# Kernel tuning notes

Measured on AMD Instinct MI355X. Metric: run time of the kernel, lower is better.

The kernel has to match this reference:

```python
import jax, jax.numpy as jnp
import numpy as np

EMBD_DIM = 768
NUM_HEADS = 12
DEPTH = EMBD_DIM // NUM_HEADS


def setup_inputs() -> dict:
    key = jax.random.key(0)
    ks = jax.random.split(key, 8)
    B, S, D = 4, 2048, EMBD_DIM
    scale = 1.0 / np.sqrt(D)
    return {
        "q": jax.random.normal(ks[0], (B, S, D), dtype=jnp.float32),
        "k": jax.random.normal(ks[1], (B, S, D), dtype=jnp.float32),
        "v": jax.random.normal(ks[2], (B, S, D), dtype=jnp.float32),
        # torch nn.Linear stores weight as [out, in]; y = x @ W.T
        "wq": jax.random.normal(ks[3], (D, D), dtype=jnp.float32) * scale,
        "wk": jax.random.normal(ks[4], (D, D), dtype=jnp.float32) * scale,
        "wv": jax.random.normal(ks[5], (D, D), dtype=jnp.float32) * scale,
        "wd": jax.random.normal(ks[6], (D, D), dtype=jnp.float32) * scale,
        "bd": jax.random.normal(ks[7], (D,), dtype=jnp.float32) * 0.01,
    }


def _split_heads(x):
    B, S, _ = x.shape
    return x.reshape(B, S, NUM_HEADS, DEPTH).transpose(0, 2, 1, 3)  # [B,H,S,depth]


def reference(q, k, v, wq, wk, wv, wd, bd):
    B, S, D = q.shape
    qh = _split_heads(q @ wq.T)
    kh = _split_heads(k @ wk.T)
    vh = _split_heads(v @ wv.T)
    scale = jnp.sqrt(jnp.float32(DEPTH))
    logits = jnp.einsum("bhqd,bhkd->bhqk", qh, kh) / scale  # [B,H,S,S]
    attn = jax.nn.softmax(logits, axis=-1)
    ctx = jnp.einsum("bhqk,bhkd->bhqd", attn, vh)
    ctx = ctx.transpose(0, 2, 1, 3).reshape(B, S, D)
    out = ctx @ wd.T + bd
    return out, attn[:, 0, :, :]
```

## Files before the change

kernel.cpp:

```cpp
#include <hip/hip_runtime.h>
#include <stdint.h>

typedef unsigned short u16;
typedef __attribute__((ext_vector_type(8))) __bf16 bf16x8;
typedef __attribute__((ext_vector_type(4))) float f32x4;

#define BSD 6291456
#define WSZ 589824

__device__ __forceinline__ u16 f2bf(float f) {
  union { float f; uint32_t u; } v; v.f = f;
  return (u16)((v.u + 0x7fff + ((v.u >> 16) & 1)) >> 16);
}

__device__ __forceinline__ void load_lds16(const u16* g, u16* l) {
  __builtin_amdgcn_global_load_lds((__attribute__((address_space(1))) void*)(void*)g,
                                   (__attribute__((address_space(3))) void*)l, 16, 0, 0);
}

__device__ __forceinline__ f32x4 mfma16(bf16x8 a, bf16x8 b, f32x4 c) {
  return __builtin_amdgcn_mfma_f32_16x16x32_bf16(a, b, c, 0, 0, 0);
}

__global__ void convert_all(const float* __restrict__ q, const float* __restrict__ k,
                            const float* __restrict__ v, const float* __restrict__ wq,
                            const float* __restrict__ wk, const float* __restrict__ wv,
                            const float* __restrict__ wd, u16* __restrict__ ws) {
  long e = ((long)blockIdx.x * blockDim.x + threadIdx.x) * 8;
  const float* src;
  if (e < (long)BSD) src = q + e;
  else if (e < 2L*BSD) src = k + (e - (long)BSD);
  else if (e < 3L*BSD) src = v + (e - 2L*BSD);
  else {
    long r = e - 3L*BSD;
    if (r < (long)WSZ) src = wq + r;
    else if (r < 2L*WSZ) src = wk + (r - (long)WSZ);
    else if (r < 3L*WSZ) src = wv + (r - 2L*WSZ);
    else src = wd + (r - 3L*WSZ);
  }
  float4 f0 = ((const float4*)src)[0];
  float4 f1 = ((const float4*)src)[1];
  union { u16 s[8]; uint4 u; } o;
  o.s[0]=f2bf(f0.x); o.s[1]=f2bf(f0.y); o.s[2]=f2bf(f0.z); o.s[3]=f2bf(f0.w);
  o.s[4]=f2bf(f1.x); o.s[5]=f2bf(f1.y); o.s[6]=f2bf(f1.z); o.s[7]=f2bf(f1.w);
  *(uint4*)(ws + e) = o.u;
}

template<int OUTF32>
__global__ __launch_bounds__(256) void gemm_bt(const u16* __restrict__ A, const u16* __restrict__ Bm,
                                               u16* __restrict__ Cb, float* __restrict__ Cf,
                                               const float* __restrict__ bias, int M, int N, int K) {
  __shared__ u16 ldsA[128*32];
  __shared__ u16 ldsB[128*32];
  const int t = threadIdx.x, w = t >> 6, lane = t & 63, quad = lane >> 4, n16 = lane & 15;
  const int m0 = blockIdx.x * 128, n0 = blockIdx.y * 128;
  const int wr = (w >> 1) * 64, wc = (w & 1) * 64;
  f32x4 acc[4][4] = {};
  for (int k0 = 0; k0 < K; k0 += 32) {
    __syncthreads();
#pragma unroll
    for (int j = 0; j < 2; ++j) {
      int slot = j*256 + w*64 + lane;
      int row = slot >> 2, ch = slot & 3;
      load_lds16(A  + (size_t)(m0 + row)*K + k0 + ch*8, ldsA + slot*8);
      load_lds16(Bm + (size_t)(n0 + row)*K + k0 + ch*8, ldsB + slot*8);
    }
    __syncthreads();
    bf16x8 af[4], bf[4];
#pragma unroll
    for (int i = 0; i < 4; ++i) {
      af[i] = *(const bf16x8*)(ldsA + (wr + i*16 + n16)*32 + quad*8);
      bf[i] = *(const bf16x8*)(ldsB + (wc + i*16 + n16)*32 + quad*8);
    }
#pragma unroll
    for (int mi = 0; mi < 4; ++mi)
#pragma unroll
      for (int ni = 0; ni < 4; ++ni)
        acc[mi][ni] = mfma16(af[mi], bf[ni], acc[mi][ni]);
  }
#pragma unroll
  for (int mi = 0; mi < 4; ++mi)
#pragma unroll
    for (int ni = 0; ni < 4; ++ni)
#pragma unroll
      for (int i = 0; i < 4; ++i) {
        size_t r = (size_t)m0 + wr + mi*16 + quad*4 + i;
        size_t c = (size_t)n0 + wc + ni*16 + n16;
        float val = acc[mi][ni][i];
        if (OUTF32) Cf[r*(size_t)N + c] = val + bias[c];
        else        Cb[r*(size_t)N + c] = f2bf(val);
      }
}

__global__ __launch_bounds__(256) void transpose_v(const u16* __restrict__ Vh, u16* __restrict__ Vt) {
  __shared__ u16 tile[64][72];
  const int b = blockIdx.z, h = blockIdx.y, st = blockIdx.x;
  const int t = threadIdx.x;
#pragma unroll
  for (int i = 0; i < 16; ++i) {
    int e = i*256 + t;
    int s = e >> 6, d = e & 63;
    tile[s][d] = Vh[(size_t)(b*2048 + st*64 + s)*768 + h*64 + d];
  }
  __syncthreads();
#pragma unroll
  for (int i = 0; i < 16; ++i) {
    int e = i*256 + t;
    int d = e >> 6, s = e & 63;
    Vt[((size_t)(b*12 + h)*64 + d)*2048 + st*64 + s] = tile[s][d];
  }
}

__global__ __launch_bounds__(256) void attn_fused(const u16* __restrict__ Qh, const u16* __restrict__ Kh,
                                                  const u16* __restrict__ Vt, u16* __restrict__ ctx,
                                                  float* __restrict__ rowsum) {
  __shared__ u16 ldsK[128*64];
  __shared__ u16 ldsV[64*128];
  __shared__ u16 ldsP[128*128];
  const int qt = blockIdx.x, h = blockIdx.y, b = blockIdx.z;
  const int t = threadIdx.x, w = t >> 6, lane = t & 63, quad = lane >> 4, n16 = lane & 15;
  const int q0 = qt * 128;
  const u16* Kbh = Kh + (size_t)b*2048*768 + h*64;
  const u16* Vbh = Vt + (size_t)(b*12 + h)*64*2048;
  bf16x8 qf[2][2];
#pragma unroll
  for (int mi = 0; mi < 2; ++mi)
#pragma unroll
    for (int ks = 0; ks < 2; ++ks)
      qf[mi][ks] = *(const bf16x8*)(Qh + (size_t)(b*2048 + q0 + w*32 + mi*16 + n16)*768
                                       + h*64 + ks*32 + quad*8);
  f32x4 oacc[2][4] = {};
  float rs[2][4] = {};
#pragma unroll 1
  for (int c = 0; c < 16; ++c) {
    __syncthreads();
#pragma unroll
    for (int j = 0; j < 4; ++j) {
      int slot = j*256 + w*64 + lane;
      { int n = slot >> 3, cs = slot & 7, cg = cs ^ (n & 7);
        load_lds16(Kbh + (size_t)(c*128 + n)*768 + cg*8, ldsK + slot*8); }
      { int d = slot >> 4, cs = slot & 15, cg = cs ^ (d & 15);
        load_lds16(Vbh + (size_t)d*2048 + c*128 + cg*8, ldsV + slot*8); }
    }
    __syncthreads();
    f32x4 sacc[2][8] = {};
#pragma unroll
    for (int ni = 0; ni < 8; ++ni) {
      int n = ni*16 + n16;
      bf16x8 kf0 = *(const bf16x8*)(ldsK + n*64 + ((quad)     ^ (n & 7))*8);
      bf16x8 kf1 = *(const bf16x8*)(ldsK + n*64 + ((4 + quad) ^ (n & 7))*8);
#pragma unroll
      for (int mi = 0; mi < 2; ++mi) {
        sacc[mi][ni] = mfma16(qf[mi][0], kf0, sacc[mi][ni]);
        sacc[mi][ni] = mfma16(qf[mi][1], kf1, sacc[mi][ni]);
      }
    }
#pragma unroll
    for (int mi = 0; mi < 2; ++mi)
#pragma unroll
      for (int ni = 0; ni < 8; ++ni)
#pragma unroll
        for (int i = 0; i < 4; ++i) {
          float p = __expf(sacc[mi][ni][i] * 0.125f);
          rs[mi][i] += p;
          int m = w*32 + mi*16 + quad*4 + i;
          int n = ni*16 + n16;
          ldsP[m*128 + (((n >> 3) ^ (m & 7)) * 8) + (n & 7)] = f2bf(p);
        }
    __syncthreads();
#pragma unroll
    for (int ks = 0; ks < 4; ++ks) {
      bf16x8 pf[2], vf[4];
#pragma unroll
      for (int mi = 0; mi < 2; ++mi) {
        int m = w*32 + mi*16 + n16;
        pf[mi] = *(const bf16x8*)(ldsP + m*128 + (((ks*4 + quad) ^ (m & 7)) * 8));
      }
#pragma unroll
      for (int di = 0; di < 4; ++di) {
        int n = di*16 + n16;
        vf[di] = *(const bf16x8*)(ldsV + n*128 + (((ks*4 + quad) ^ (n & 15)) * 8));
      }
#pragma unroll
      for (int mi = 0; mi < 2; ++mi)
#pragma unroll
        for (int di = 0; di < 4; ++di)
          oacc[mi][di] = mfma16(pf[mi], vf[di], oacc[mi][di]);
    }
  }
#pragma unroll
  for (int mi = 0; mi < 2; ++mi)
#pragma unroll
    for (int i = 0; i < 4; ++i) {
      float s = rs[mi][i];
      s += __shfl_xor(s, 1); s += __shfl_xor(s, 2);
      s += __shfl_xor(s, 4); s += __shfl_xor(s, 8);
      rs[mi][i] = s;
    }
#pragma unroll
  for (int mi = 0; mi < 2; ++mi)
#pragma unroll
    for (int di = 0; di < 4; ++di)
#pragma unroll
      for (int i = 0; i < 4; ++i) {
        size_t r = (size_t)b*2048 + q0 + w*32 + mi*16 + quad*4 + i;
        int cc = h*64 + di*16 + n16;
        ctx[r*768 + cc] = f2bf(oacc[mi][di][i] / rs[mi][i]);
      }
  if (h == 0 && n16 == 0) {
#pragma unroll
    for (int mi = 0; mi < 2; ++mi)
#pragma unroll
      for (int i = 0; i < 4; ++i)
        rowsum[b*2048 + q0 + w*32 + mi*16 + quad*4 + i] = rs[mi][i];
  }
}

__global__ __launch_bounds__(256) void attn_h0(const u16* __restrict__ Qh, const u16* __restrict__ Kh,
                                               const float* __restrict__ rowsum, float* __restrict__ aout) {
  __shared__ u16 ldsK[128*64];
  const int qt = blockIdx.x, kt = blockIdx.y, b = blockIdx.z;
  const int t = threadIdx.x, w = t >> 6, lane = t & 63, quad = lane >> 4, n16 = lane & 15;
  const int q0 = qt * 128;
  const u16* Kbh = Kh + (size_t)b*2048*768;
  bf16x8 qf[2][2];
#pragma unroll
  for (int mi = 0; mi < 2; ++mi)
#pragma unroll
    for (int ks = 0; ks < 2; ++ks)
      qf[mi][ks] = *(const bf16x8*)(Qh + (size_t)(b*2048 + q0 + w*32 + mi*16 + n16)*768
                                       + ks*32 + quad*8);
#pragma unroll
  for (int j = 0; j < 4; ++j) {
    int slot = j*256 + w*64 + lane;
    int n = slot >> 3, cs = slot & 7, cg = cs ^ (n & 7);
    load_lds16(Kbh + (size_t)(kt*128 + n)*768 + cg*8, ldsK + slot*8);
  }
  __syncthreads();
  f32x4 sacc[2][8] = {};
#pragma unroll
  for (int ni = 0; ni < 8; ++ni) {
    int n = ni*16 + n16;
    bf16x8 kf0 = *(const bf16x8*)(ldsK + n*64 + ((quad)     ^ (n & 7))*8);
    bf16x8 kf1 = *(const bf16x8*)(ldsK + n*64 + ((4 + quad) ^ (n & 7))*8);
#pragma unroll
    for (int mi = 0; mi < 2; ++mi) {
      sacc[mi][ni] = mfma16(qf[mi][0], kf0, sacc[mi][ni]);
      sacc[mi][ni] = mfma16(qf[mi][1], kf1, sacc[mi][ni]);
    }
  }
  float inv[2][4];
#pragma unroll
  for (int mi = 0; mi < 2; ++mi)
#pragma unroll
    for (int i = 0; i < 4; ++i)
      inv[mi][i] = 1.0f / rowsum[b*2048 + q0 + w*32 + mi*16 + quad*4 + i];
#pragma unroll
  for (int mi = 0; mi < 2; ++mi)
#pragma unroll
    for (int ni = 0; ni < 8; ++ni)
#pragma unroll
      for (int i = 0; i < 4; ++i) {
        size_t r = (size_t)b*2048 + q0 + w*32 + mi*16 + quad*4 + i;
        size_t cc = (size_t)kt*128 + ni*16 + n16;
        aout[r*2048 + cc] = __expf(sacc[mi][ni][i] * 0.125f) * inv[mi][i];
      }
}

extern "C" void kernel_launch(void* const* d_in, const int* in_sizes, int n_in,
                              void* d_out, int out_size, void* d_ws, size_t ws_size,
                              hipStream_t stream) {
  (void)in_sizes; (void)n_in; (void)out_size; (void)ws_size;
  const float* q  = (const float*)d_in[0];
  const float* k  = (const float*)d_in[1];
  const float* v  = (const float*)d_in[2];
  const float* wq = (const float*)d_in[3];
  const float* wk = (const float*)d_in[4];
  const float* wv = (const float*)d_in[5];
  const float* wd = (const float*)d_in[6];
  const float* bd = (const float*)d_in[7];

  u16* ws  = (u16*)d_ws;
  u16* qb  = ws;
  u16* kb  = ws + (size_t)BSD;
  u16* vb  = ws + 2L*BSD;
  u16* wqb = ws + 3L*BSD;
  u16* wkb = wqb + WSZ;
  u16* wvb = wqb + 2L*WSZ;
  u16* wdb = wqb + 3L*WSZ;
  u16* Qh  = ws + 3L*BSD + 4L*WSZ;
  u16* Kh  = Qh + (size_t)BSD;
  float* rsum = (float*)(Kh + (size_t)BSD);
  u16* Vh  = kb;
  u16* Vt  = qb;
  u16* ctx = vb;
  float* out  = (float*)d_out;
  float* aout = out + (size_t)BSD;

  convert_all<<<dim3(10368), 256, 0, stream>>>(q, k, v, wq, wk, wv, wd, ws);
  dim3 gp(64, 6);
  gemm_bt<0><<<gp, 256, 0, stream>>>(qb, wqb, Qh, nullptr, nullptr, 8192, 768, 768);
  gemm_bt<0><<<gp, 256, 0, stream>>>(kb, wkb, Kh, nullptr, nullptr, 8192, 768, 768);
  gemm_bt<0><<<gp, 256, 0, stream>>>(vb, wvb, Vh, nullptr, nullptr, 8192, 768, 768);
  transpose_v<<<dim3(32, 12, 4), 256, 0, stream>>>(Vh, Vt);
  attn_fused<<<dim3(16, 12, 4), 256, 0, stream>>>(Qh, Kh, Vt, ctx, rsum);
  attn_h0<<<dim3(16, 16, 4), 256, 0, stream>>>(Qh, Kh, rsum, aout);
  gemm_bt<1><<<gp, 256, 0, stream>>>(ctx, wdb, nullptr, out, bd, 8192, 768, 768);
}
```

Before: 375.3 us.

## Shrink attention KV tile to 64, transpose S MFMA, pack P stores

Halves the key/value tile per iteration from 128 to 64 columns. This cuts LDS use from about 64KB to 32KB and sets launch bounds to 4 blocks per CU to raise occupancy. It swaps the MFMA operand order so each lane holds four consecutive key columns of one query row, which allows packed 8-byte P writes to LDS and one row-sum accumulator per row. The change also uses exp2f with a prescaled constant and reciprocal multiplication in the epilogue. In exchange there are twice as many loop iterations and barriers, and the row sums need an extra shuffle to redistribute them.

```diff
diff --git a/kernel.cpp b/kernel.cpp
--- a/kernel.cpp
+++ b/kernel.cpp
@@ -111,15 +111,16 @@
   }
 }
 
-__global__ __launch_bounds__(256) void attn_fused(const u16* __restrict__ Qh, const u16* __restrict__ Kh,
-                                                  const u16* __restrict__ Vt, u16* __restrict__ ctx,
-                                                  float* __restrict__ rowsum) {
-  __shared__ u16 ldsK[128*64];
-  __shared__ u16 ldsV[64*128];
-  __shared__ u16 ldsP[128*128];
+__global__ __launch_bounds__(256, 4) void attn_fused(const u16* __restrict__ Qh, const u16* __restrict__ Kh,
+                                                     const u16* __restrict__ Vt, u16* __restrict__ ctx,
+                                                     float* __restrict__ rowsum) {
+  __shared__ u16 ldsK[64*64];
+  __shared__ u16 ldsV[64*64];
+  __shared__ u16 ldsP[128*64];
   const int qt = blockIdx.x, h = blockIdx.y, b = blockIdx.z;
   const int t = threadIdx.x, w = t >> 6, lane = t & 63, quad = lane >> 4, n16 = lane & 15;
   const int q0 = qt * 128;
+  const int sw = n16 & 7;
   const u16* Kbh = Kh + (size_t)b*2048*768 + h*64;
   const u16* Vbh = Vt + (size_t)(b*12 + h)*64*2048;
   bf16x8 qf[2][2];
@@ -130,57 +131,58 @@
       qf[mi][ks] = *(const bf16x8*)(Qh + (size_t)(b*2048 + q0 + w*32 + mi*16 + n16)*768
                                        + h*64 + ks*32 + quad*8);
   f32x4 oacc[2][4] = {};
-  float rs[2][4] = {};
+  float rs[2] = {};
+  const float escale = 0.18033688f;
 #pragma unroll 1
-  for (int c = 0; c < 16; ++c) {
+  for (int c = 0; c < 32; ++c) {
     __syncthreads();
 #pragma unroll
-    for (int j = 0; j < 4; ++j) {
-      int slot = j*256 + w*64 + lane;
-      { int n = slot >> 3, cs = slot & 7, cg = cs ^ (n & 7);
-        load_lds16(Kbh + (size_t)(c*128 + n)*768 + cg*8, ldsK + slot*8); }
-      { int d = slot >> 4, cs = slot & 15, cg = cs ^ (d & 15);
-        load_lds16(Vbh + (size_t)d*2048 + c*128 + cg*8, ldsV + slot*8); }
+    for (int j = 0; j < 2; ++j) {
+      int slot = j*256 + t;
+      int n = slot >> 3, cg = (slot & 7) ^ (n & 7);
+      load_lds16(Kbh + (size_t)(c*64 + n)*768 + cg*8, ldsK + slot*8);
+      load_lds16(Vbh + (size_t)n*2048 + c*64 + cg*8, ldsV + slot*8);
     }
     __syncthreads();
-    f32x4 sacc[2][8] = {};
-#pragma unroll
-    for (int ni = 0; ni < 8; ++ni) {
-      int n = ni*16 + n16;
-      bf16x8 kf0 = *(const bf16x8*)(ldsK + n*64 + ((quad)     ^ (n & 7))*8);
-      bf16x8 kf1 = *(const bf16x8*)(ldsK + n*64 + ((4 + quad) ^ (n & 7))*8);
+    f32x4 sacc[4][2] = {};
+#pragma unroll
+    for (int ni = 0; ni < 4; ++ni) {
+      const u16* krow = ldsK + (ni*16 + n16)*64;
+      bf16x8 kf0 = *(const bf16x8*)(krow + ((0 + quad) ^ sw)*8);
+      bf16x8 kf1 = *(const bf16x8*)(krow + ((4 + quad) ^ sw)*8);
 #pragma unroll
       for (int mi = 0; mi < 2; ++mi) {
-        sacc[mi][ni] = mfma16(qf[mi][0], kf0, sacc[mi][ni]);
-        sacc[mi][ni] = mfma16(qf[mi][1], kf1, sacc[mi][ni]);
-      }
-    }
-#pragma unroll
-    for (int mi = 0; mi < 2; ++mi)
-#pragma unroll
-      for (int ni = 0; ni < 8; ++ni)
-#pragma unroll
-        for (int i = 0; i < 4; ++i) {
-          float p = __expf(sacc[mi][ni][i] * 0.125f);
-          rs[mi][i] += p;
-          int m = w*32 + mi*16 + quad*4 + i;
-          int n = ni*16 + n16;
-          ldsP[m*128 + (((n >> 3) ^ (m & 7)) * 8) + (n & 7)] = f2bf(p);
-        }
-    __syncthreads();
-#pragma unroll
-    for (int ks = 0; ks < 4; ++ks) {
+        sacc[ni][mi] = mfma16(kf0, qf[mi][0], sacc[ni][mi]);
+        sacc[ni][mi] = mfma16(kf1, qf[mi][1], sacc[ni][mi]);
+      }
+    }
+#pragma unroll
+    for (int mi = 0; mi < 2; ++mi) {
+      int m = w*32 + mi*16 + n16;
+      u16* prow = ldsP + m*64 + (quad & 1)*4;
+#pragma unroll
+      for (int ni = 0; ni < 4; ++ni) {
+        float p0 = exp2f(sacc[ni][mi][0] * escale);
+        float p1 = exp2f(sacc[ni][mi][1] * escale);
+        float p2 = exp2f(sacc[ni][mi][2] * escale);
+        float p3 = exp2f(sacc[ni][mi][3] * escale);
+        rs[mi] += (p0 + p1) + (p2 + p3);
+        uint2 pk;
+        pk.x = (uint32_t)f2bf(p0) | ((uint32_t)f2bf(p1) << 16);
+        pk.y = (uint32_t)f2bf(p2) | ((uint32_t)f2bf(p3) << 16);
+        int c128 = ((ni*2 + (quad >> 1)) ^ sw);
+        *(uint2*)(prow + c128*8) = pk;
+      }
+    }
+#pragma unroll
+    for (int kt = 0; kt < 2; ++kt) {
       bf16x8 pf[2], vf[4];
 #pragma unroll
-      for (int mi = 0; mi < 2; ++mi) {
-        int m = w*32 + mi*16 + n16;
-        pf[mi] = *(const bf16x8*)(ldsP + m*128 + (((ks*4 + quad) ^ (m & 7)) * 8));
-      }
-#pragma unroll
-      for (int di = 0; di < 4; ++di) {
-        int n = di*16 + n16;
-        vf[di] = *(const bf16x8*)(ldsV + n*128 + (((ks*4 + quad) ^ (n & 15)) * 8));
-      }
+      for (int mi = 0; mi < 2; ++mi)
+        pf[mi] = *(const bf16x8*)(ldsP + (w*32 + mi*16 + n16)*64 + ((kt*4 + quad) ^ sw)*8);
+#pragma unroll
+      for (int di = 0; di < 4; ++di)
+        vf[di] = *(const bf16x8*)(ldsV + (di*16 + n16)*64 + ((kt*4 + quad) ^ sw)*8);
 #pragma unroll
       for (int mi = 0; mi < 2; ++mi)
 #pragma unroll
@@ -189,14 +191,18 @@
     }
   }
 #pragma unroll
-  for (int mi = 0; mi < 2; ++mi)
-#pragma unroll
-    for (int i = 0; i < 4; ++i) {
-      float s = rs[mi][i];
-      s += __shfl_xor(s, 1); s += __shfl_xor(s, 2);
-      s += __shfl_xor(s, 4); s += __shfl_xor(s, 8);
-      rs[mi][i] = s;
-    }
+  for (int mi = 0; mi < 2; ++mi) {
+    float s = rs[mi];
+    s += __shfl_xor(s, 16);
+    s += __shfl_xor(s, 32);
+    rs[mi] = s;
+  }
+  float invr[2][4];
+#pragma unroll
+  for (int mi = 0; mi < 2; ++mi)
+#pragma unroll
+    for (int i = 0; i < 4; ++i)
+      invr[mi][i] = 1.0f / __shfl(rs[mi], (lane & 48) | (quad*4 + i));
 #pragma unroll
   for (int mi = 0; mi < 2; ++mi)
 #pragma unroll
@@ -205,14 +211,12 @@
       for (int i = 0; i < 4; ++i) {
         size_t r = (size_t)b*2048 + q0 + w*32 + mi*16 + quad*4 + i;
         int cc = h*64 + di*16 + n16;
-        ctx[r*768 + cc] = f2bf(oacc[mi][di][i] / rs[mi][i]);
-      }
-  if (h == 0 && n16 == 0) {
+        ctx[r*768 + cc] = f2bf(oacc[mi][di][i] * invr[mi][i]);
+      }
+  if (h == 0 && quad == 0) {
 #pragma unroll
     for (int mi = 0; mi < 2; ++mi)
-#pragma unroll
-      for (int i = 0; i < 4; ++i)
-        rowsum[b*2048 + q0 + w*32 + mi*16 + quad*4 + i] = rs[mi][i];
+      rowsum[b*2048 + q0 + w*32 + mi*16 + n16] = rs[mi];
   }
 }
 
```

Result: faster. 366.0 us (-2.5%).
